# Kernel tuning notes

Measured on AMD Instinct MI355X. Metric: run time of the kernel, lower is better.

The kernel has to match this reference:

```python
import jax, jax.numpy as jnp
import numpy as np

N_HEADS = 16
ROPE_THETA = 10000.0


def setup_inputs() -> dict:
    key = jax.random.key(0)
    ks = jax.random.split(key, 6)
    B, T, D = 2, 2048, 1024
    hd = D // N_HEADS
    x = jax.random.normal(ks[0], (B, T, D), dtype=jnp.float32)
    # Linear weights (torch nn.Linear weight layout: (out, in)), scaled like kaiming-ish init
    s = 1.0 / np.sqrt(D)
    wq = jax.random.normal(ks[1], (D, D), dtype=jnp.float32) * s
    wk = jax.random.normal(ks[2], (D, D), dtype=jnp.float32) * s
    wv = jax.random.normal(ks[3], (D, D), dtype=jnp.float32) * s
    wo = jax.random.normal(ks[4], (D, D), dtype=jnp.float32) * s
    # RoPE freqs_cis as real (T, hd//2, 2) = (cos, sin)
    inv_freq = 1.0 / (ROPE_THETA ** (jnp.arange(0, hd, 2, dtype=jnp.float32) / hd))  # (hd//2,)
    angles = jnp.arange(T, dtype=jnp.float32)[:, None] * inv_freq[None, :]  # (T, hd//2)
    freqs_cis = jnp.stack([jnp.cos(angles), jnp.sin(angles)], axis=-1)  # (T, hd//2, 2)
    # Additive causal mask (large negative above diagonal)
    neg = jnp.float32(-1e9)
    causal_mask = jnp.where(jnp.tril(jnp.ones((T, T), dtype=bool)), jnp.float32(0.0), neg)
    return {"x": x, "wq": wq, "wk": wk, "wv": wv, "wo": wo,
            "freqs_cis": freqs_cis, "causal_mask": causal_mask}


def _apply_rotary(q, k, freqs_cis):
    # q, k: (B, H, T, hd); freqs_cis: (T, hd//2, 2) with (cos, sin)
    B, H, T, hd = q.shape
    cos = freqs_cis[:, :, 0][None, None]  # (1,1,T,hd//2)
    sin = freqs_cis[:, :, 1][None, None]

    def rot(t):
        tr = t.reshape(B, H, T, hd // 2, 2)
        t0, t1 = tr[..., 0], tr[..., 1]
        o0 = t0 * cos - t1 * sin
        o1 = t0 * sin + t1 * cos
        return jnp.stack([o0, o1], axis=-1).reshape(B, H, T, hd)

    return rot(q), rot(k)


def reference(x, wq, wk, wv, wo, freqs_cis, causal_mask):
    B, T, D = x.shape
    H = N_HEADS
    hd = D // H
    scale = hd ** -0.5
    # Projections (torch Linear: x @ W.T), reshape to (B, H, T, hd)
    q = (x @ wq.T).reshape(B, T, H, hd).transpose(0, 2, 1, 3)
    k = (x @ wk.T).reshape(B, T, H, hd).transpose(0, 2, 1, 3)
    v = (x @ wv.T).reshape(B, T, H, hd).transpose(0, 2, 1, 3)
    q, k = _apply_rotary(q, k, freqs_cis[:T])
    attn = jnp.einsum('bhqd,bhkd->bhqk', q, k) * scale + causal_mask[:T, :T]
    p = jax.nn.softmax(attn, axis=-1)
    out = jnp.einsum('bhqk,bhkd->bhqd', p, v)
    out = out.transpose(0, 2, 1, 3).reshape(B, T, D)
    return out @ wo.T
```

## Files before the change

### kernel.cpp

```cpp
#include <hip/hip_runtime.h>
#include <hip/hip_bf16.h>

#define T_SEQ 2048
#define DMODEL 1024
#define NH 16
#define HD 64

typedef __attribute__((ext_vector_type(8))) short bf16x8;
typedef __attribute__((ext_vector_type(4))) float f32x4;
typedef __attribute__((ext_vector_type(16))) float f32x16;

__device__ __forceinline__ f32x4 mfma16(bf16x8 a, bf16x8 b, f32x4 c) {
  return __builtin_amdgcn_mfma_f32_16x16x32_bf16(a, b, c, 0, 0, 0);
}
__device__ __forceinline__ f32x16 mfma32(bf16x8 a, bf16x8 b, f32x16 c) {
  return __builtin_amdgcn_mfma_f32_32x32x16_bf16(a, b, c, 0, 0, 0);
}

__device__ __forceinline__ unsigned short f2b(float f) {
  return __builtin_bit_cast(unsigned short, __float2bfloat16(f));
}
__device__ __forceinline__ unsigned packpair(float lo, float hi) {
  return (unsigned)f2b(lo) | ((unsigned)f2b(hi) << 16);
}

#define GLOAD16(g, l)                                                          \
  __builtin_amdgcn_global_load_lds(                                            \
      (const __attribute__((address_space(1))) unsigned int*)(g),              \
      (__attribute__((address_space(3))) unsigned int*)(l), 16, 0, 0)

#define PLSWAP(a, b) asm("v_permlane32_swap_b32 %0, %1" : "+v"(a), "+v"(b))

#define VMCNT0_BAR()                                                           \
  do {                                                                         \
    asm volatile("s_waitcnt vmcnt(0)" ::: "memory");                           \
    __builtin_amdgcn_s_barrier();                                              \
  } while (0)

#define QSCALE 0.125f

__global__ __launch_bounds__(256)
void cvt_all(const float* __restrict__ x,  const float* __restrict__ wq,
             const float* __restrict__ wk, const float* __restrict__ wv,
             const float* __restrict__ wo, unsigned short* __restrict__ xb,
             unsigned short* __restrict__ wqkv, unsigned short* __restrict__ wob) {
  const int g = blockIdx.x * 256 + threadIdx.x;
  const int M1 = 1 << 20, WG = 1 << 18;
  const float* src; unsigned short* dst; int off;
  if (g < M1)               { src = x;  dst = xb;             off = g; }
  else if (g < M1 + WG)     { src = wq; dst = wqkv;           off = g - M1; }
  else if (g < M1 + 2 * WG) { src = wk; dst = wqkv + M1;      off = g - M1 - WG; }
  else if (g < M1 + 3 * WG) { src = wv; dst = wqkv + 2 * M1;  off = g - M1 - 2 * WG; }
  else                      { src = wo; dst = wob;            off = g - M1 - 3 * WG; }
  const float4 v = ((const float4*)src)[off];
  ushort4 o;
  o.x = f2b(v.x); o.y = f2b(v.y); o.z = f2b(v.z); o.w = f2b(v.w);
  ((ushort4*)dst)[off] = o;
}

template<int AMODE, int CMODE>
__global__ __launch_bounds__(256)
void gemm_bf16(const unsigned short* __restrict__ A, const unsigned short* __restrict__ B,
               unsigned short* __restrict__ Cq, unsigned short* __restrict__ Cv,
               float* __restrict__ Cf, const float* __restrict__ fcg,
               int M, int N, int K) {
  __shared__ __align__(16) unsigned short As[2][4096];
  __shared__ __align__(16) unsigned short Bs[2][4096];
  const int tid  = threadIdx.x;
  const int wid  = tid >> 6, lane = tid & 63;
  const int lg   = lane >> 4, lr = lane & 15;
  const int wr   = wid >> 1, wc = wid & 1;
  const int m0   = blockIdx.y * 128, n0 = blockIdx.x * 128;

  auto stage = [&](unsigned short* asb, unsigned short* bsb, int k0) {
    #pragma unroll
    for (int i = 0; i < 2; ++i) {
      const int c = i * 256 + wid * 64 + lane;
      const int r = c >> 2, slot = c & 3, js = slot ^ (r & 3);
      const unsigned short* ga;
      if (AMODE == 0) ga = A + (m0 + r) * K + k0 + js * 8;
      else {
        const int m = m0 + r;
        ga = A + (((m >> 11) * NH + (k0 >> 6)) * T_SEQ + (m & 2047)) * HD + (k0 & 63) + js * 8;
      }
      GLOAD16(ga, (char*)asb + i * 4096 + wid * 1024);
      GLOAD16(B + (n0 + r) * K + k0 + js * 8, (char*)bsb + i * 4096 + wid * 1024);
    }
  };

  f32x4 acc[4][4];
  const f32x4 z = {0.f, 0.f, 0.f, 0.f};
  #pragma unroll
  for (int i = 0; i < 4; ++i)
    #pragma unroll
    for (int j = 0; j < 4; ++j) acc[i][j] = z;

  const int KT = K >> 5;
  stage(As[0], Bs[0], 0);
  VMCNT0_BAR();
  int cur = 0;
  for (int t = 0; t < KT; ++t) {
    if (t + 1 < KT) stage(As[cur ^ 1], Bs[cur ^ 1], (t + 1) * 32);

    bf16x8 af[4], bfr[4];
    #pragma unroll
    for (int f = 0; f < 4; ++f) {
      const int ra = wr * 64 + f * 16 + lr;
      af[f]  = *(const bf16x8*)((const char*)As[cur] + ra * 64 + ((lg ^ (ra & 3)) << 4));
      const int rb = wc * 64 + f * 16 + lr;
      bfr[f] = *(const bf16x8*)((const char*)Bs[cur] + rb * 64 + ((lg ^ (rb & 3)) << 4));
    }
    #pragma unroll
    for (int i = 0; i < 4; ++i)
      #pragma unroll
      for (int j = 0; j < 4; ++j)
        acc[i][j] = mfma16(af[i], bfr[j], acc[i][j]);

    VMCNT0_BAR();
    cur ^= 1;
  }

  #pragma unroll
  for (int i = 0; i < 4; ++i)
    #pragma unroll
    for (int j = 0; j < 4; ++j)
      #pragma unroll
      for (int reg = 0; reg < 4; ++reg) {
        const int m = m0 + wr * 64 + i * 16 + lg * 4 + reg;
        const int n = n0 + wc * 64 + j * 16 + lr;
        const float val = acc[i][j][reg];
        if (CMODE == 0) {
          Cf[m * N + n] = val;
        } else {
          const int b = m >> 11, t = m & 2047;
          if (n < 2048) {
            const float pv = __shfl_xor(val, 1);
            const int d = n & 63;
            const float co = fcg[t * 64 + (d & 62)];
            const float si = fcg[t * 64 + (d & 62) + 1];
            float outv = (d & 1) ? (pv * si + val * co) : (val * co - pv * si);
            if (n < 1024) outv *= QSCALE;
            const int head = (n & 1023) >> 6;
            Cq[(n >> 10) * 4194304 + ((b * NH + head) * T_SEQ + t) * HD + d] = f2b(outv);
          } else {
            const int nv = n - 2048, head = nv >> 6, d = nv & 63;
            Cv[((b * NH + head) * HD + d) * T_SEQ + t] = f2b(val);
          }
        }
      }
}

__global__ __launch_bounds__(256)
void attn_kernel(const unsigned short* __restrict__ Q, const unsigned short* __restrict__ K,
                 const unsigned short* __restrict__ V, unsigned short* __restrict__ AO) {
  __shared__ __align__(16) char Ks[8192];
  __shared__ __align__(16) char Vs[8192];
  const int tid = threadIdx.x;
  const int wid = tid >> 6, lane = tid & 63;
  const int l31 = lane & 31, hi = lane >> 5;

  const int id  = blockIdx.x;
  const int xcd = id & 7, j = id >> 3;
  const int bh  = xcd * 4 + (j & 3);
  const int qb  = (j < 32) ? (15 - (j >> 2)) : ((j >> 2) - 8);
  const int base = bh * (T_SEQ * HD);
  const int qw  = qb * 128 + wid * 32;
  const int q   = qw + l31;

  bf16x8 qfr[4];
  #pragma unroll
  for (int ds = 0; ds < 4; ++ds)
    qfr[ds] = *(const bf16x8*)(Q + base + q * HD + ds * 16 + hi * 8);

  f32x16 o[2];
  #pragma unroll
  for (int r = 0; r < 16; ++r) { o[0][r] = 0.f; o[1][r] = 0.f; }
  float m_run = -1e30f, l_run = 0.f;

  const int ntiles = 2 * qb + 2;
  for (int kt = 0; kt < ntiles; ++kt) {
    const int k0 = kt * 64;
    __syncthreads();
    #pragma unroll
    for (int i = 0; i < 2; ++i) {
      const int c = i * 256 + wid * 64 + lane;
      const int r = c >> 3, sg = c & 7, js = sg ^ (r & 7);
      GLOAD16(K + base + (k0 + r) * HD + js * 8, Ks + i * 4096 + wid * 1024);
      GLOAD16(V + base + r * T_SEQ + k0 + js * 8, Vs + i * 4096 + wid * 1024);
    }
    __syncthreads();

    if (k0 <= qw + 31) {
      f32x16 s0, s1;
      #pragma unroll
      for (int r = 0; r < 16; ++r) { s0[r] = 0.f; s1[r] = 0.f; }
      #pragma unroll
      for (int ds = 0; ds < 4; ++ds) {
        const int sg = ds * 2 + hi;
        const int key0 = l31, key1 = 32 + l31;
        const bf16x8 kf0 = *(const bf16x8*)(Ks + key0 * 128 + ((sg ^ (key0 & 7)) << 4));
        const bf16x8 kf1 = *(const bf16x8*)(Ks + key1 * 128 + ((sg ^ (key1 & 7)) << 4));
        s0 = mfma32(kf0, qfr[ds], s0);
        s1 = mfma32(kf1, qfr[ds], s1);
      }

      if (k0 + 63 > qw) {
        #pragma unroll
        for (int r = 0; r < 16; ++r) {
          const int kr = (r & 3) + 8 * (r >> 2) + 4 * hi;
          if (k0 + kr > q)      s0[r] = -1e30f;
          if (k0 + 32 + kr > q) s1[r] = -1e30f;
        }
      }

      float mx = s0[0];
      #pragma unroll
      for (int r = 1; r < 16; ++r) mx = fmaxf(mx, s0[r]);
      #pragma unroll
      for (int r = 0; r < 16; ++r) mx = fmaxf(mx, s1[r]);
      mx = fmaxf(mx, __shfl_xor(mx, 32));
      if (!__all(mx <= m_run + 8.0f)) {
        const float mnew = fmaxf(m_run, mx);
        const float alpha = __expf(m_run - mnew);
        m_run = mnew;
        l_run *= alpha;
        #pragma unroll
        for (int r = 0; r < 16; ++r) { o[0][r] *= alpha; o[1][r] *= alpha; }
      }
      float sumA = 0.f, sumB = 0.f;
      #pragma unroll
      for (int r = 0; r < 16; ++r) {
        s0[r] = __expf(s0[r] - m_run); sumA += s0[r];
        s1[r] = __expf(s1[r] - m_run); sumB += s1[r];
      }
      float sum = sumA + sumB;
      sum += __shfl_xor(sum, 32);
      l_run += sum;

      #pragma unroll
      for (int ks = 0; ks < 4; ++ks) {
        const f32x16 pt = (ks < 2) ? s0 : s1;
        const int m = 8 * (ks & 1);
        unsigned wA = packpair(pt[m + 0], pt[m + 1]);
        unsigned wB = packpair(pt[m + 2], pt[m + 3]);
        unsigned wC = packpair(pt[m + 4], pt[m + 5]);
        unsigned wD = packpair(pt[m + 6], pt[m + 7]);
        PLSWAP(wA, wC);
        PLSWAP(wB, wD);
        uint4 uw; uw.x = wA; uw.y = wB; uw.z = wC; uw.w = wD;
        const bf16x8 pf = __builtin_bit_cast(bf16x8, uw);
        #pragma unroll
        for (int db = 0; db < 2; ++db) {
          const int d = db * 32 + l31;
          const int sg = ks * 2 + hi;
          const bf16x8 vf = *(const bf16x8*)(Vs + d * 128 + ((sg ^ (d & 7)) << 4));
          o[db] = mfma32(vf, pf, o[db]);
        }
      }
    }
  }

  const float inv = 1.f / l_run;
  #pragma unroll
  for (int db = 0; db < 2; ++db)
    #pragma unroll
    for (int t = 0; t < 4; ++t) {
      ushort4 pk;
      pk.x = f2b(o[db][4 * t + 0] * inv);
      pk.y = f2b(o[db][4 * t + 1] * inv);
      pk.z = f2b(o[db][4 * t + 2] * inv);
      pk.w = f2b(o[db][4 * t + 3] * inv);
      const int d = db * 32 + 8 * t + 4 * hi;
      *(ushort4*)(AO + base + q * HD + d) = pk;
    }
}

extern "C" void kernel_launch(void* const* d_in, const int* in_sizes, int n_in,
                              void* d_out, int out_size, void* d_ws, size_t ws_size,
                              hipStream_t stream) {
  const float* x  = (const float*)d_in[0];
  const float* wq = (const float*)d_in[1];
  const float* wk = (const float*)d_in[2];
  const float* wv = (const float*)d_in[3];
  const float* wo = (const float*)d_in[4];
  const float* fc = (const float*)d_in[5];
  float* out = (float*)d_out;

  const int ME = 1 << 20;
  unsigned short* W    = (unsigned short*)d_ws;
  unsigned short* xb   = W;
  unsigned short* wqkv = W + 4 * ME;
  unsigned short* wob  = W + 7 * ME;
  unsigned short* Qb   = W + 8 * ME;
  unsigned short* Kb   = W + 12 * ME;
  unsigned short* Vt   = W + 16 * ME;
  unsigned short* AO   = W + 20 * ME;

  hipLaunchKernelGGL(cvt_all, dim3(8192), dim3(256), 0, stream,
                     x, wq, wk, wv, wo, xb, wqkv, wob);

  hipLaunchKernelGGL((gemm_bf16<0, 3>), dim3(24, 32), dim3(256), 0, stream,
                     xb, wqkv, Qb, Vt, (float*)nullptr, fc, 4096, 3072, 1024);

  hipLaunchKernelGGL(attn_kernel, dim3(512), dim3(256), 0, stream, Qb, Kb, Vt, AO);

  hipLaunchKernelGGL((gemm_bf16<1, 0>), dim3(8, 32), dim3(256), 0, stream,
                     AO, wob, (unsigned short*)nullptr, (unsigned short*)nullptr,
                     out, (const float*)nullptr, 4096, 1024, 1024);
}
```

Before: 229.8 us.

## Double-buffer K/V tiles in attention and rework GEMM LDS swizzle

The attention kernel moves from a single K/V LDS buffer, loaded and waited on every tile, to two buffers. The next tile's global-to-LDS loads are issued right after the barrier, so they overlap the current tile's QK, softmax and PV math. The GEMM drops its explicit vmcnt(0)+barrier macro and uses one __syncthreads at the top of each iteration, relying on the compiler's release fence to drain outstanding loads. It also changes the LDS XOR swizzle from (r&3) to ((r>>1)&3) to cut bank conflicts on the 64-byte rows. The cost is twice the attention LDS footprint, which may lower occupancy, and a reliance on __syncthreads waiting for the LDS-direct loads.

```diff
diff --git a/kernel.cpp b/kernel.cpp
--- a/kernel.cpp
+++ b/kernel.cpp
@@ -30,12 +30,6 @@
       (__attribute__((address_space(3))) unsigned int*)(l), 16, 0, 0)
 
 #define PLSWAP(a, b) asm("v_permlane32_swap_b32 %0, %1" : "+v"(a), "+v"(b))
-
-#define VMCNT0_BAR()                                                           \
-  do {                                                                         \
-    asm volatile("s_waitcnt vmcnt(0)" ::: "memory");                           \
-    __builtin_amdgcn_s_barrier();                                              \
-  } while (0)
 
 #define QSCALE 0.125f
 
@@ -72,19 +66,20 @@
   const int wr   = wid >> 1, wc = wid & 1;
   const int m0   = blockIdx.y * 128, n0 = blockIdx.x * 128;
 
-  auto stage = [&](unsigned short* asb, unsigned short* bsb, int k0) {
+  auto stage = [&](int buf, int k0) {
     #pragma unroll
     for (int i = 0; i < 2; ++i) {
       const int c = i * 256 + wid * 64 + lane;
-      const int r = c >> 2, slot = c & 3, js = slot ^ (r & 3);
+      const int r = c >> 2, slot = c & 3;
+      const int js = slot ^ ((r >> 1) & 3);
       const unsigned short* ga;
       if (AMODE == 0) ga = A + (m0 + r) * K + k0 + js * 8;
       else {
         const int m = m0 + r;
         ga = A + (((m >> 11) * NH + (k0 >> 6)) * T_SEQ + (m & 2047)) * HD + (k0 & 63) + js * 8;
       }
-      GLOAD16(ga, (char*)asb + i * 4096 + wid * 1024);
-      GLOAD16(B + (n0 + r) * K + k0 + js * 8, (char*)bsb + i * 4096 + wid * 1024);
+      GLOAD16(ga, (char*)As[buf] + i * 4096 + wid * 1024);
+      GLOAD16(B + (n0 + r) * K + k0 + js * 8, (char*)Bs[buf] + i * 4096 + wid * 1024);
     }
   };
 
@@ -96,27 +91,25 @@
     for (int j = 0; j < 4; ++j) acc[i][j] = z;
 
   const int KT = K >> 5;
-  stage(As[0], Bs[0], 0);
-  VMCNT0_BAR();
+  stage(0, 0);
   int cur = 0;
   for (int t = 0; t < KT; ++t) {
-    if (t + 1 < KT) stage(As[cur ^ 1], Bs[cur ^ 1], (t + 1) * 32);
+    __syncthreads();
+    if (t + 1 < KT) stage(cur ^ 1, (t + 1) * 32);
 
     bf16x8 af[4], bfr[4];
     #pragma unroll
     for (int f = 0; f < 4; ++f) {
       const int ra = wr * 64 + f * 16 + lr;
-      af[f]  = *(const bf16x8*)((const char*)As[cur] + ra * 64 + ((lg ^ (ra & 3)) << 4));
+      af[f]  = *(const bf16x8*)((const char*)As[cur] + ra * 64 + ((lg ^ ((ra >> 1) & 3)) << 4));
       const int rb = wc * 64 + f * 16 + lr;
-      bfr[f] = *(const bf16x8*)((const char*)Bs[cur] + rb * 64 + ((lg ^ (rb & 3)) << 4));
+      bfr[f] = *(const bf16x8*)((const char*)Bs[cur] + rb * 64 + ((lg ^ ((rb >> 1) & 3)) << 4));
     }
     #pragma unroll
     for (int i = 0; i < 4; ++i)
       #pragma unroll
       for (int j = 0; j < 4; ++j)
         acc[i][j] = mfma16(af[i], bfr[j], acc[i][j]);
-
-    VMCNT0_BAR();
     cur ^= 1;
   }
 
@@ -153,8 +146,8 @@
 __global__ __launch_bounds__(256)
 void attn_kernel(const unsigned short* __restrict__ Q, const unsigned short* __restrict__ K,
                  const unsigned short* __restrict__ V, unsigned short* __restrict__ AO) {
-  __shared__ __align__(16) char Ks[8192];
-  __shared__ __align__(16) char Vs[8192];
+  __shared__ __align__(16) char Ks[2][8192];
+  __shared__ __align__(16) char Vs[2][8192];
   const int tid = threadIdx.x;
   const int wid = tid >> 6, lane = tid & 63;
   const int l31 = lane & 31, hi = lane >> 5;
@@ -167,6 +160,16 @@
   const int qw  = qb * 128 + wid * 32;
   const int q   = qw + l31;
 
+  auto stage = [&](int buf, int k0) {
+    #pragma unroll
+    for (int i = 0; i < 2; ++i) {
+      const int c = i * 256 + wid * 64 + lane;
+      const int r = c >> 3, sg = c & 7, js = sg ^ (r & 7);
+      GLOAD16(K + base + (k0 + r) * HD + js * 8, Ks[buf] + i * 4096 + wid * 1024);
+      GLOAD16(V + base + r * T_SEQ + k0 + js * 8, Vs[buf] + i * 4096 + wid * 1024);
+    }
+  };
+
   bf16x8 qfr[4];
   #pragma unroll
   for (int ds = 0; ds < 4; ++ds)
@@ -178,19 +181,16 @@
   float m_run = -1e30f, l_run = 0.f;
 
   const int ntiles = 2 * qb + 2;
+  stage(0, 0);
+  int cur = 0;
   for (int kt = 0; kt < ntiles; ++kt) {
     const int k0 = kt * 64;
     __syncthreads();
-    #pragma unroll
-    for (int i = 0; i < 2; ++i) {
-      const int c = i * 256 + wid * 64 + lane;
-      const int r = c >> 3, sg = c & 7, js = sg ^ (r & 7);
-      GLOAD16(K + base + (k0 + r) * HD + js * 8, Ks + i * 4096 + wid * 1024);
-      GLOAD16(V + base + r * T_SEQ + k0 + js * 8, Vs + i * 4096 + wid * 1024);
-    }
-    __syncthreads();
+    if (kt + 1 < ntiles) stage(cur ^ 1, (kt + 1) * 64);
 
     if (k0 <= qw + 31) {
+      const char* Kc = Ks[cur];
+      const char* Vc = Vs[cur];
       f32x16 s0, s1;
       #pragma unroll
       for (int r = 0; r < 16; ++r) { s0[r] = 0.f; s1[r] = 0.f; }
@@ -198,8 +198,8 @@
       for (int ds = 0; ds < 4; ++ds) {
         const int sg = ds * 2 + hi;
         const int key0 = l31, key1 = 32 + l31;
-        const bf16x8 kf0 = *(const bf16x8*)(Ks + key0 * 128 + ((sg ^ (key0 & 7)) << 4));
-        const bf16x8 kf1 = *(const bf16x8*)(Ks + key1 * 128 + ((sg ^ (key1 & 7)) << 4));
+        const bf16x8 kf0 = *(const bf16x8*)(Kc + key0 * 128 + ((sg ^ (key0 & 7)) << 4));
+        const bf16x8 kf1 = *(const bf16x8*)(Kc + key1 * 128 + ((sg ^ (key1 & 7)) << 4));
         s0 = mfma32(kf0, qfr[ds], s0);
         s1 = mfma32(kf1, qfr[ds], s1);
       }
@@ -253,11 +253,12 @@
         for (int db = 0; db < 2; ++db) {
           const int d = db * 32 + l31;
           const int sg = ks * 2 + hi;
-          const bf16x8 vf = *(const bf16x8*)(Vs + d * 128 + ((sg ^ (d & 7)) << 4));
+          const bf16x8 vf = *(const bf16x8*)(Vc + d * 128 + ((sg ^ (d & 7)) << 4));
           o[db] = mfma32(vf, pf, o[db]);
         }
       }
     }
+    cur ^= 1;
   }
 
   const float inv = 1.f / l_run;
```

New measurement: 230.1 us. Within noise of the previous version (+0.2%).
